# Performance work log

Measured on AMD Instinct MI355X. Metric: run time of the kernel, lower is better.

Reference implementation:

```python
import jax, jax.numpy as jnp
import numpy as np

SCALE = 0.02

def setup_inputs() -> dict:
    key = jax.random.key(0)
    k1, k2 = jax.random.split(key)
    B, D, T, H = 2, 1024, 2048, 16
    x = jax.random.normal(k1, (B, D, T), dtype=jnp.float32)
    qkv = jax.random.normal(k2, (3, H, D, D // H), dtype=jnp.float32) * SCALE
    return {"x": x, "qkv": qkv}

def reference(x, qkv):
    B, D, T = x.shape
    H = qkv.shape[1]
    # fused QKV projection: (B,D,T) x (3,H,D,Dh) -> (3,B,H,T,Dh)
    proj = jnp.einsum('bdt,nhdD->nbhtD', x, qkv)
    q, k, v = proj[0], proj[1], proj[2]
    scale = jnp.sqrt(jnp.asarray(D // H, dtype=x.dtype))
    # scores: (B,H,T,T)
    attn = jax.nn.softmax(jnp.einsum('bhtD,bhTD->bhtT', q, k) / scale, axis=-1)
    # weighted values, head dim placed before time: (B,H,Dh,T)
    out = jnp.einsum('bhtT,bhTD->bhDt', attn, v)
    return out.reshape(B, D, T)
```

## Files before the change

kernel.cpp:

```cpp
#include <hip/hip_runtime.h>

#define B_ 2
#define D_ 1024
#define T_ 2048
#define H_ 16
#define DH_ 64
#define BH_ (B_ * H_)

typedef __attribute__((ext_vector_type(8))) short bf16x8;
typedef __attribute__((ext_vector_type(8))) unsigned short u16x8;
typedef __attribute__((ext_vector_type(4))) float f32x4;

__device__ __forceinline__ unsigned short f2bf(float f) {
    unsigned u = __float_as_uint(f);
    u += 0x7fffu + ((u >> 16) & 1u);
    return (unsigned short)(u >> 16);
}

__global__ __launch_bounds__(256) void xpose_kernel(
    const float* __restrict__ x, unsigned short* __restrict__ xT)
{
    __shared__ __align__(16) unsigned short Ls[64][68];
    const int t0 = blockIdx.x * 64;
    const int d0 = blockIdx.y * 64;
    const int b  = blockIdx.z;
    const int tid = threadIdx.x;

    const float* xb = x + (size_t)b * D_ * T_ + (size_t)d0 * T_ + t0;
    #pragma unroll
    for (int p = 0; p < 4; p++) {
        int i4  = tid + p * 256;
        int row = i4 >> 4;
        int c4  = (i4 & 15) << 2;
        float4 v = *(const float4*)(xb + (size_t)row * T_ + c4);
        ushort4 u;
        u.x = f2bf(v.x); u.y = f2bf(v.y); u.z = f2bf(v.z); u.w = f2bf(v.w);
        *(ushort4*)&Ls[row][c4] = u;
    }
    __syncthreads();
    unsigned short* ob = xT + (size_t)b * T_ * D_ + (size_t)t0 * D_ + d0;
    #pragma unroll
    for (int p = 0; p < 2; p++) {
        int i    = tid + p * 256;
        int orow = i >> 3;
        int oc8  = (i & 7) * 8;
        u16x8 tv;
        #pragma unroll
        for (int j = 0; j < 8; j++) tv[j] = Ls[oc8 + j][orow];
        *(u16x8*)(ob + (size_t)orow * D_ + oc8) = tv;
    }
}

__global__ __launch_bounds__(256) void wpose_kernel(
    const float* __restrict__ w, unsigned short* __restrict__ wT)
{
    __shared__ __align__(16) unsigned short Ls[64][68];
    const int d0 = blockIdx.x * 64;
    const int nh = blockIdx.y;
    const int tid = threadIdx.x;

    const float* wb = w + (size_t)nh * D_ * DH_ + (size_t)d0 * DH_;
    #pragma unroll
    for (int p = 0; p < 4; p++) {
        int i4  = tid + p * 256;
        int row = i4 >> 4;
        int c4  = (i4 & 15) << 2;
        float4 v = *(const float4*)(wb + (size_t)row * DH_ + c4);
        ushort4 u;
        u.x = f2bf(v.x); u.y = f2bf(v.y); u.z = f2bf(v.z); u.w = f2bf(v.w);
        *(ushort4*)&Ls[row][c4] = u;
    }
    __syncthreads();
    unsigned short* ob = wT + (size_t)nh * DH_ * D_ + d0;
    #pragma unroll
    for (int p = 0; p < 2; p++) {
        int i    = tid + p * 256;
        int orow = i >> 3;
        int oc8  = (i & 7) * 8;
        u16x8 tv;
        #pragma unroll
        for (int j = 0; j < 8; j++) tv[j] = Ls[oc8 + j][orow];
        *(u16x8*)(ob + (size_t)orow * D_ + oc8) = tv;
    }
}

#define LX 72

__global__ __launch_bounds__(256) void proj_mfma_kernel(
    const unsigned short* __restrict__ xT, const unsigned short* __restrict__ wT,
    unsigned short* __restrict__ qk, unsigned short* __restrict__ vT)
{
    __shared__ __align__(16) unsigned short Buf[18432];
    unsigned short* Xs = Buf;
    unsigned short* Ws = Buf + 9216;
    unsigned short* Es = Buf;

    const int t0 = blockIdx.x * 128;
    const int y  = blockIdx.y;
    const int n  = y >> 4;
    const int b  = (y >> 3) & 1;
    const int hp = y & 7;

    const unsigned short* xb = xT + (size_t)b * T_ * D_ + (size_t)t0 * D_;
    const unsigned short* wb = wT + (size_t)(n * 16 + 2 * hp) * DH_ * D_;

    const int tid  = threadIdx.x;
    const int wv   = tid >> 6;
    const int lane = tid & 63;
    const int c15  = lane & 15;
    const int quad = lane >> 4;
    const int tq   = (wv & 1) * 64;
    const int dq   = (wv >> 1) * 64;

    f32x4 acc[4][4];
    #pragma unroll
    for (int mt = 0; mt < 4; mt++)
        #pragma unroll
        for (int nt = 0; nt < 4; nt++)
            acc[mt][nt] = (f32x4){0.f, 0.f, 0.f, 0.f};

    for (int k0 = 0; k0 < D_; k0 += 64) {
        __syncthreads();
        #pragma unroll
        for (int p = 0; p < 4; p++) {
            int i    = tid + p * 256;
            int row  = i >> 3;
            int col8 = (i & 7) * 8;
            *(u16x8*)&Xs[row * LX + col8] =
                *(const u16x8*)(xb + (size_t)row * D_ + k0 + col8);
            *(u16x8*)&Ws[row * LX + col8] =
                *(const u16x8*)(wb + (size_t)row * D_ + k0 + col8);
        }
        __syncthreads();

        bf16x8 af[4][2], bf[4][2];
        #pragma unroll
        for (int mt = 0; mt < 4; mt++)
            #pragma unroll
            for (int s = 0; s < 2; s++)
                af[mt][s] = *(bf16x8*)&Xs[(tq + mt * 16 + c15) * LX + quad * 8 + s * 32];
        #pragma unroll
        for (int nt = 0; nt < 4; nt++)
            #pragma unroll
            for (int s = 0; s < 2; s++)
                bf[nt][s] = *(bf16x8*)&Ws[(dq + nt * 16 + c15) * LX + quad * 8 + s * 32];

        #pragma unroll
        for (int mt = 0; mt < 4; mt++)
            #pragma unroll
            for (int nt = 0; nt < 4; nt++)
                #pragma unroll
                for (int s = 0; s < 2; s++)
                    acc[mt][nt] = __builtin_amdgcn_mfma_f32_16x16x32_bf16(
                        af[mt][s], bf[nt][s], acc[mt][nt], 0, 0, 0);
    }

    const float scale = (n == 0) ? 0.125f : 1.0f;
    __syncthreads();
    #pragma unroll
    for (int mt = 0; mt < 4; mt++)
        #pragma unroll
        for (int nt = 0; nt < 4; nt++)
            #pragma unroll
            for (int r = 0; r < 4; r++)
                Es[(tq + mt * 16 + quad * 4 + r) * 136 + dq + nt * 16 + c15] =
                    f2bf(acc[mt][nt][r] * scale);
    __syncthreads();

    if (n < 2) {
        #pragma unroll
        for (int p = 0; p < 8; p++) {
            int i    = tid + p * 256;
            int row  = i >> 4;
            int col8 = (i & 15) * 8;
            int head = col8 >> 6;
            unsigned short* ob = qk +
                ((size_t)(n * 32 + b * 16 + 2 * hp + head) * T_ + t0 + row) * DH_ + (col8 & 63);
            *(u16x8*)ob = *(u16x8*)&Es[row * 136 + col8];
        }
    } else {
        #pragma unroll
        for (int p = 0; p < 8; p++) {
            int i    = tid + p * 256;
            int orow = i >> 4;
            int oc8  = (i & 15) * 8;
            int head = orow >> 6;
            u16x8 tv;
            #pragma unroll
            for (int j = 0; j < 8; j++) tv[j] = Es[(oc8 + j) * 136 + orow];
            unsigned short* ob = vT +
                (size_t)(b * 16 + 2 * hp + head) * DH_ * T_ +
                (size_t)(orow & 63) * T_ + t0 + oc8;
            *(u16x8*)ob = tv;
        }
    }
}

#define LQ 72

__global__ __launch_bounds__(256, 4) void attn_mfma_kernel(
    const unsigned short* __restrict__ qk, const unsigned short* __restrict__ vT,
    float* __restrict__ out)
{
    __shared__ __align__(16) unsigned short Sm[13824];
    unsigned short* Ks  = Sm;
    unsigned short* Vs  = Sm + 4608;
    unsigned short* Psb = Sm + 9216;

    const int flat = blockIdx.x;
    const int bh   = (flat & 7) * 4 + ((flat >> 3) >> 5);
    const int t0   = ((flat >> 3) & 31) * 64;

    const unsigned short* qg = qk + ((size_t)bh * T_ + t0) * DH_;
    const unsigned short* kg = qk + ((size_t)(BH_ + bh) * T_) * DH_;
    const unsigned short* vg = vT + (size_t)bh * DH_ * T_;

    const int tid  = threadIdx.x;
    const int wv   = tid >> 6;
    const int lane = tid & 63;
    const int c15  = lane & 15;
    const int quad = lane >> 4;

    unsigned short* Ps = Psb + wv * 1152;

    bf16x8 bq[2];
    #pragma unroll
    for (int s = 0; s < 2; s++)
        bq[s] = *(const bf16x8*)(qg + (size_t)(wv * 16 + c15) * DH_ + quad * 8 + s * 32);

    float lsum = 0.f;
    f32x4 Oacc[4];
    #pragma unroll
    for (int nt = 0; nt < 4; nt++) Oacc[nt] = (f32x4){0.f, 0.f, 0.f, 0.f};

    for (int tau = 0; tau < T_; tau += 64) {
        __syncthreads();
        #pragma unroll
        for (int p = 0; p < 2; p++) {
            int i    = tid + p * 256;
            int row  = i >> 3;
            int col8 = (i & 7) * 8;
            *(u16x8*)&Ks[row * LQ + col8] =
                *(const u16x8*)(kg + (size_t)(tau + row) * DH_ + col8);
            *(u16x8*)&Vs[row * LQ + col8] =
                *(const u16x8*)(vg + (size_t)row * T_ + tau + col8);
        }
        __syncthreads();

        #pragma unroll
        for (int mt = 0; mt < 4; mt++) {
            f32x4 sa = (f32x4){0.f, 0.f, 0.f, 0.f};
            #pragma unroll
            for (int s = 0; s < 2; s++) {
                bf16x8 ak = *(bf16x8*)&Ks[(mt * 16 + c15) * LQ + quad * 8 + s * 32];
                sa = __builtin_amdgcn_mfma_f32_16x16x32_bf16(ak, bq[s], sa, 0, 0, 0);
            }
            float p0 = __expf(sa[0]);
            float p1 = __expf(sa[1]);
            float p2 = __expf(sa[2]);
            float p3 = __expf(sa[3]);
            lsum += (p0 + p1) + (p2 + p3);
            uint2 pk;
            pk.x = (unsigned)f2bf(p0) | ((unsigned)f2bf(p1) << 16);
            pk.y = (unsigned)f2bf(p2) | ((unsigned)f2bf(p3) << 16);
            *(uint2*)&Ps[c15 * LQ + mt * 16 + quad * 4] = pk;
        }

        #pragma unroll
        for (int s = 0; s < 2; s++) {
            bf16x8 ap = *(bf16x8*)&Ps[c15 * LQ + quad * 8 + s * 32];
            #pragma unroll
            for (int nt = 0; nt < 4; nt++) {
                bf16x8 bv = *(bf16x8*)&Vs[(nt * 16 + c15) * LQ + quad * 8 + s * 32];
                Oacc[nt] = __builtin_amdgcn_mfma_f32_16x16x32_bf16(ap, bv, Oacc[nt], 0, 0, 0);
            }
        }
    }

    lsum += __shfl_xor(lsum, 16);
    lsum += __shfl_xor(lsum, 32);
    float linv[4];
    #pragma unroll
    for (int r = 0; r < 4; r++)
        linv[r] = 1.0f / __shfl(lsum, quad * 4 + r);

    __syncthreads();
    float* Osw = (float*)((char*)(void*)Sm + wv * 4608);
    #pragma unroll
    for (int nt = 0; nt < 4; nt++)
        #pragma unroll
        for (int r = 0; r < 4; r++)
            Osw[(nt * 16 + c15) * 17 + quad * 4 + r] = Oacc[nt][r] * linv[r];

    const int b = bh >> 4, h = bh & 15;
    float* og = out + (size_t)b * D_ * T_ + (size_t)(h * DH_) * T_ + t0 + wv * 16;
    #pragma unroll
    for (int p = 0; p < 4; p++) {
        int idx = lane + p * 64;
        int dh  = idx >> 2;
        int qs  = (idx & 3) * 4;
        float4 v = *(float4*)&Osw[dh * 17 + qs];
        *(float4*)(og + (size_t)dh * T_ + qs) = v;
    }
}

extern "C" void kernel_launch(void* const* d_in, const int* in_sizes, int n_in,
                              void* d_out, int out_size, void* d_ws, size_t ws_size,
                              hipStream_t stream)
{
    const float* x = (const float*)d_in[0];
    const float* w = (const float*)d_in[1];
    float* out = (float*)d_out;

    unsigned short* qk = (unsigned short*)d_ws;
    unsigned short* vT = (unsigned short*)((char*)d_ws + (24u << 20));
    unsigned short* xT = (unsigned short*)((char*)d_ws + (32u << 20));
    unsigned short* wT = (unsigned short*)((char*)d_ws + (40u << 20));

    xpose_kernel<<<dim3(T_ / 64, D_ / 64, B_), 256, 0, stream>>>(x, xT);
    wpose_kernel<<<dim3(D_ / 64, 3 * H_), 256, 0, stream>>>(w, wT);
    proj_mfma_kernel<<<dim3(T_ / 128, 48), 256, 0, stream>>>(xT, wT, qk, vT);
    attn_mfma_kernel<<<1024, 256, 0, stream>>>(qk, vT, out);
}
```

Before: 186.9 us.

## Register-prefetch next tiles and double-buffer swizzled LDS in projection and attention

Both the projection and attention kernels now load the next K-chunk from global memory into registers while the current chunk is being computed. The attention kernel also double-buffers its K/V tiles in LDS, dropping one barrier per iteration. It replaces padded rows with an XOR-swizzled layout for K, V and P to avoid bank conflicts. The aim is to hide global load latency behind the MFMA work, at the cost of more registers and LDS per block, which may reduce occupancy.

Measured after the change: 173.6 us. 7.1% less time.

```diff
diff --git a/kernel.cpp b/kernel.cpp
--- a/kernel.cpp
+++ b/kernel.cpp
@@ -84,15 +84,15 @@
     }
 }
 
-#define LX 72
-
-__global__ __launch_bounds__(256) void proj_mfma_kernel(
+#define LX 80
+
+__global__ __launch_bounds__(256, 3) void proj_mfma_kernel(
     const unsigned short* __restrict__ xT, const unsigned short* __restrict__ wT,
     unsigned short* __restrict__ qk, unsigned short* __restrict__ vT)
 {
-    __shared__ __align__(16) unsigned short Buf[18432];
+    __shared__ __align__(16) unsigned short Buf[20480];
     unsigned short* Xs = Buf;
-    unsigned short* Ws = Buf + 9216;
+    unsigned short* Ws = Buf + 10240;
     unsigned short* Es = Buf;
 
     const int t0 = blockIdx.x * 128;
@@ -112,6 +112,9 @@
     const int tq   = (wv & 1) * 64;
     const int dq   = (wv >> 1) * 64;
 
+    const int srow = tid >> 3;
+    const int scol = (tid & 7) * 8;
+
     f32x4 acc[4][4];
     #pragma unroll
     for (int mt = 0; mt < 4; mt++)
@@ -119,19 +122,32 @@
         for (int nt = 0; nt < 4; nt++)
             acc[mt][nt] = (f32x4){0.f, 0.f, 0.f, 0.f};
 
+    u16x8 xreg[4], wreg[4];
+    #pragma unroll
+    for (int p = 0; p < 4; p++) {
+        int row = srow + p * 32;
+        xreg[p] = *(const u16x8*)(xb + (size_t)row * D_ + scol);
+        wreg[p] = *(const u16x8*)(wb + (size_t)row * D_ + scol);
+    }
+
     for (int k0 = 0; k0 < D_; k0 += 64) {
         __syncthreads();
         #pragma unroll
         for (int p = 0; p < 4; p++) {
-            int i    = tid + p * 256;
-            int row  = i >> 3;
-            int col8 = (i & 7) * 8;
-            *(u16x8*)&Xs[row * LX + col8] =
-                *(const u16x8*)(xb + (size_t)row * D_ + k0 + col8);
-            *(u16x8*)&Ws[row * LX + col8] =
-                *(const u16x8*)(wb + (size_t)row * D_ + k0 + col8);
+            int row = srow + p * 32;
+            *(u16x8*)&Xs[row * LX + scol] = xreg[p];
+            *(u16x8*)&Ws[row * LX + scol] = wreg[p];
         }
         __syncthreads();
+
+        if (k0 + 64 < D_) {
+            #pragma unroll
+            for (int p = 0; p < 4; p++) {
+                int row = srow + p * 32;
+                xreg[p] = *(const u16x8*)(xb + (size_t)row * D_ + k0 + 64 + scol);
+                wreg[p] = *(const u16x8*)(wb + (size_t)row * D_ + k0 + 64 + scol);
+            }
+        }
 
         bf16x8 af[4][2], bf[4][2];
         #pragma unroll
@@ -196,16 +212,11 @@
     }
 }
 
-#define LQ 72
-
 __global__ __launch_bounds__(256, 4) void attn_mfma_kernel(
     const unsigned short* __restrict__ qk, const unsigned short* __restrict__ vT,
     float* __restrict__ out)
 {
-    __shared__ __align__(16) unsigned short Sm[13824];
-    unsigned short* Ks  = Sm;
-    unsigned short* Vs  = Sm + 4608;
-    unsigned short* Psb = Sm + 9216;
+    __shared__ __align__(16) unsigned short Sm[20480];
 
     const int flat = blockIdx.x;
     const int bh   = (flat & 7) * 4 + ((flat >> 3) >> 5);
@@ -220,8 +231,14 @@
     const int lane = tid & 63;
     const int c15  = lane & 15;
     const int quad = lane >> 4;
-
-    unsigned short* Ps = Psb + wv * 1152;
+    const int swz  = (c15 & 7) * 8;
+    const int h7   = c15 & 7;
+
+    unsigned short* Ps = Sm + 16384 + wv * 1024;
+
+    const int srow = tid >> 3;
+    const int sch  = tid & 7;
+    const int ssw  = ((sch ^ (srow & 7)) * 8);
 
     bf16x8 bq[2];
     #pragma unroll
@@ -233,26 +250,43 @@
     #pragma unroll
     for (int nt = 0; nt < 4; nt++) Oacc[nt] = (f32x4){0.f, 0.f, 0.f, 0.f};
 
+    u16x8 kreg[2], vreg[2];
+    #pragma unroll
+    for (int p = 0; p < 2; p++) {
+        int row = srow + p * 32;
+        kreg[p] = *(const u16x8*)(kg + (size_t)row * DH_ + sch * 8);
+        vreg[p] = *(const u16x8*)(vg + (size_t)row * T_ + sch * 8);
+    }
+    #pragma unroll
+    for (int p = 0; p < 2; p++) {
+        int row = srow + p * 32;
+        *(u16x8*)&Sm[row * 64 + ssw]        = kreg[p];
+        *(u16x8*)&Sm[4096 + row * 64 + ssw] = vreg[p];
+    }
+
     for (int tau = 0; tau < T_; tau += 64) {
+        const int cur = (tau >> 6) & 1;
+        unsigned short* Ks = Sm + cur * 8192;
+        unsigned short* Vs = Ks + 4096;
         __syncthreads();
-        #pragma unroll
-        for (int p = 0; p < 2; p++) {
-            int i    = tid + p * 256;
-            int row  = i >> 3;
-            int col8 = (i & 7) * 8;
-            *(u16x8*)&Ks[row * LQ + col8] =
-                *(const u16x8*)(kg + (size_t)(tau + row) * DH_ + col8);
-            *(u16x8*)&Vs[row * LQ + col8] =
-                *(const u16x8*)(vg + (size_t)row * T_ + tau + col8);
-        }
-        __syncthreads();
+
+        const bool pf = (tau + 64 < T_);
+        if (pf) {
+            #pragma unroll
+            for (int p = 0; p < 2; p++) {
+                int row = srow + p * 32;
+                kreg[p] = *(const u16x8*)(kg + (size_t)(tau + 64 + row) * DH_ + sch * 8);
+                vreg[p] = *(const u16x8*)(vg + (size_t)row * T_ + tau + 64 + sch * 8);
+            }
+        }
 
         #pragma unroll
         for (int mt = 0; mt < 4; mt++) {
             f32x4 sa = (f32x4){0.f, 0.f, 0.f, 0.f};
             #pragma unroll
             for (int s = 0; s < 2; s++) {
-                bf16x8 ak = *(bf16x8*)&Ks[(mt * 16 + c15) * LQ + quad * 8 + s * 32];
+                bf16x8 ak = *(bf16x8*)&Ks[(mt * 16 + c15) * 64 +
+                                          (((quad + 4 * s) ^ h7) * 8)];
                 sa = __builtin_amdgcn_mfma_f32_16x16x32_bf16(ak, bq[s], sa, 0, 0, 0);
             }
             float p0 = __expf(sa[0]);
@@ -263,16 +297,27 @@
             uint2 pk;
             pk.x = (unsigned)f2bf(p0) | ((unsigned)f2bf(p1) << 16);
             pk.y = (unsigned)f2bf(p2) | ((unsigned)f2bf(p3) << 16);
-            *(uint2*)&Ps[c15 * LQ + mt * 16 + quad * 4] = pk;
+            *(uint2*)&Ps[c15 * 64 + ((mt * 16 + quad * 4) ^ swz)] = pk;
         }
 
         #pragma unroll
         for (int s = 0; s < 2; s++) {
-            bf16x8 ap = *(bf16x8*)&Ps[c15 * LQ + quad * 8 + s * 32];
+            bf16x8 ap = *(bf16x8*)&Ps[c15 * 64 + ((quad * 8 + s * 32) ^ swz)];
             #pragma unroll
             for (int nt = 0; nt < 4; nt++) {
-                bf16x8 bv = *(bf16x8*)&Vs[(nt * 16 + c15) * LQ + quad * 8 + s * 32];
+                bf16x8 bv = *(bf16x8*)&Vs[(nt * 16 + c15) * 64 +
+                                          (((quad + 4 * s) ^ h7) * 8)];
                 Oacc[nt] = __builtin_amdgcn_mfma_f32_16x16x32_bf16(ap, bv, Oacc[nt], 0, 0, 0);
+            }
+        }
+
+        if (pf) {
+            unsigned short* Kn = Sm + (1 - cur) * 8192;
+            #pragma unroll
+            for (int p = 0; p < 2; p++) {
+                int row = srow + p * 32;
+                *(u16x8*)&Kn[row * 64 + ssw]        = kreg[p];
+                *(u16x8*)&Kn[4096 + row * 64 + ssw] = vreg[p];
             }
         }
     }
@@ -285,7 +330,7 @@
         linv[r] = 1.0f / __shfl(lsum, quad * 4 + r);
 
     __syncthreads();
-    float* Osw = (float*)((char*)(void*)Sm + wv * 4608);
+    float* Osw = (float*)(void*)Sm + wv * 1088;
     #pragma unroll
     for (int nt = 0; nt < 4; nt++)
         #pragma unroll
```
